# Optimization experiments

Measured on AMD Instinct MI355X. Metric: run time of the kernel, lower is better.

## Reference

```python
import jax, jax.numpy as jnp
import numpy as np

V, E, H, T = 50000, 1024, 1024, 128
L, MAXL = 50, 50
PAD, O_TOK = 0, 1


def setup_inputs() -> dict:
    key = jax.random.key(0)
    ks = jax.random.split(key, 18)
    s = 0.05
    f = lambda k, shape: jax.random.normal(k, shape, jnp.float32) * s
    return {
        'input_ids': jax.random.randint(ks[0], (1, L), 1, V),
        'tag_ids': jax.random.randint(ks[1], (1, L), 1, T),  # >=1 so no pad tags
        'word_embed': f(ks[2], (V, E)),
        'enc_Wih': f(ks[3], (3 * H, E)),
        'enc_Whh': f(ks[4], (3 * H, H)),
        'enc_bih': f(ks[5], (3 * H,)),
        'enc_bhh': f(ks[6], (3 * H,)),
        'dec_embed': f(ks[7], (T, H)),
        'attn_W': f(ks[8], (MAXL, 2 * H)),
        'attn_b': f(ks[9], (MAXL,)),
        'comb_W': f(ks[10], (H, 2 * H)),
        'comb_b': f(ks[11], (H,)),
        'dec_Wih': f(ks[12], (3 * H, H)),
        'dec_Whh': f(ks[13], (3 * H, H)),
        'dec_bih': f(ks[14], (3 * H,)),
        'dec_bhh': f(ks[15], (3 * H,)),
        'out_W': f(ks[16], (T, H)),
        'out_b': f(ks[17], (T,)),
    }


def _gru_cell(x, h, Wih, Whh, bih, bhh):
    # PyTorch GRU cell semantics
    gi = Wih @ x + bih
    gh = Whh @ h + bhh
    i_r, i_z, i_n = jnp.split(gi, 3)
    h_r, h_z, h_n = jnp.split(gh, 3)
    r = jax.nn.sigmoid(i_r + h_r)
    z = jax.nn.sigmoid(i_z + h_z)
    n = jnp.tanh(i_n + r * h_n)
    return (1.0 - z) * n + z * h


def _forward(word_embed, enc_Wih, enc_Whh, enc_bih, enc_bhh,
             dec_embed, attn_W, attn_b, comb_W, comb_b,
             dec_Wih, dec_Whh, dec_bih, dec_bhh, out_W, out_b,
             input_ids, tag_ids):
    src = input_ids[0]  # (L,)
    tgt = tag_ids[0]    # (L,)

    def enc_step(h, tok):
        h2 = _gru_cell(word_embed[tok], h, enc_Wih, enc_Whh, enc_bih, enc_bhh)
        return h2, h2

    h_enc, enc_outs = jax.lax.scan(enc_step, jnp.zeros((H,), word_embed.dtype), src)
    # enc_outs: (L, H); L == MAX_LENGTH so the buffer is fully filled

    dec_in = jnp.concatenate([jnp.array([O_TOK], tgt.dtype), tgt[:-1]])  # teacher forcing

    def dec_step(h, xt):
        tok, tgt_t = xt
        e = dec_embed[tok]  # (H,), dropout is identity in eval
        aw = jax.nn.softmax(attn_W @ jnp.concatenate([e, h]) + attn_b)  # (MAXL,)
        ctx = aw @ enc_outs  # (H,)
        o = jax.nn.relu(comb_W @ jnp.concatenate([e, ctx]) + comb_b)
        h2 = _gru_cell(o, h, dec_Wih, dec_Whh, dec_bih, dec_bhh)
        logp = jax.nn.log_softmax(out_W @ h2 + out_b)  # decoder output (log-probs)
        # original applies CrossEntropyLoss on log-probs -> log_softmax applied twice
        nll = -jax.nn.log_softmax(logp)[tgt_t]
        step_loss = jnp.where(tgt_t == PAD, jnp.zeros((), logp.dtype), nll)
        return h2, (logp, step_loss)

    _, (logps, losses) = jax.lax.scan(dec_step, h_enc, (dec_in, tgt))
    return logps, jnp.sum(losses)  # (L, T), scalar


def reference(input_ids, tag_ids, word_embed, enc_Wih, enc_Whh, enc_bih, enc_bhh,
              dec_embed, attn_W, attn_b, comb_W, comb_b,
              dec_Wih, dec_Whh, dec_bih, dec_bhh, out_W, out_b):
    return _forward(word_embed, enc_Wih, enc_Whh, enc_bih, enc_bhh,
                    dec_embed, attn_W, attn_b, comb_W, comb_b,
                    dec_Wih, dec_Whh, dec_bih, dec_bhh, out_W, out_b,
                    input_ids, tag_ids)
```

## Files before the change

### kernel.cpp

```cpp
#include <hip/hip_runtime.h>
#include <cstdint>


#define HDIM 1024
#define LSEQ 50
#define TDIM 128
#define PB   6
#define NPROD 128
#define LSTRP 65

typedef float f32x4 __attribute__((ext_vector_type(4)));
typedef _Float16 h2 __attribute__((ext_vector_type(2)));

#if __has_builtin(__builtin_amdgcn_fdot2)
#define FDOT2(a,b,c) __builtin_amdgcn_fdot2((a),(b),(c),false)
#else
__device__ __forceinline__ float fdot2_sw(h2 a, h2 b, float c){
  return c + (float)a[0]*(float)b[0] + (float)a[1]*(float)b[1];
}
#define FDOT2(a,b,c) fdot2_sw((a),(b),(c))
#endif

struct KArgs {
  const int* input_ids; const int* tag_ids;
  const float* word_embed;
  const float* enc_Wih; const float* enc_Whh; const float* enc_bih; const float* enc_bhh;
  const float* dec_embed; const float* attn_W; const float* attn_b;
  const float* comb_W; const float* comb_b;
  const float* dec_Wih; const float* dec_Whh; const float* dec_bih; const float* dec_bhh;
  const float* out_W; const float* out_b;
  float* out;
  unsigned* ctrM; unsigned* ctrO; unsigned* ctrV;
  float* hbE;
  float* hbD;
  float* obD;
  float* logits;
  float* enc_outs;
  float* attn_e;
  float* pre_comb;
  float* MT;
};

__device__ __forceinline__ void fence_vm(){
  asm volatile("s_waitcnt vmcnt(0)" ::: "memory");
}
__device__ __forceinline__ void st_coh(float* p, float v){
  __hip_atomic_store(p, v, __ATOMIC_RELAXED, __HIP_MEMORY_SCOPE_AGENT);
}
__device__ __forceinline__ void st_tag(float* p, float v, unsigned tag){
  unsigned b = (__float_as_uint(v) & ~31u) | tag;
  st_coh(p, __uint_as_float(b));
}
__device__ __forceinline__ void stf(unsigned* p, unsigned v){
  __hip_atomic_store(p, v, __ATOMIC_RELAXED, __HIP_MEMORY_SCOPE_AGENT);
}
__device__ __forceinline__ unsigned ldu(const unsigned* p){
  return __hip_atomic_load(p, __ATOMIC_RELAXED, __HIP_MEMORY_SCOPE_AGENT);
}
__device__ __forceinline__ void addc0(unsigned* base){
  __hip_atomic_fetch_add(base, 1u, __ATOMIC_RELAXED, __HIP_MEMORY_SCOPE_AGENT);
}
__device__ __forceinline__ f32x4 coh_load4(const float* p){
  f32x4 v;
  asm volatile("global_load_dwordx4 %0, %1, off sc0 sc1\n\ts_waitcnt vmcnt(0)"
               : "=v"(v) : "v"(p) : "memory");
  return v;
}

template<int N>
__device__ __forceinline__ void wred_batch(float* v){
  #pragma unroll
  for(int o=32;o>0;o>>=1){
    #pragma unroll
    for(int i=0;i<N;i++) v[i] += __shfl_xor(v[i],o,64);
  }
}
__device__ __forceinline__ float wred_sum(float v){
  #pragma unroll
  for(int o=32;o>0;o>>=1) v += __shfl_xor(v,o,64);
  return v;
}
__device__ __forceinline__ float wred_max(float v){
  #pragma unroll
  for(int o=32;o>0;o>>=1) v = fmaxf(v,__shfl_xor(v,o,64));
  return v;
}

__device__ __forceinline__ void load_vec16(const float* __restrict__ v, float* hc, int lane){
  const f32x4* p = reinterpret_cast<const f32x4*>(v) + lane*4;
  f32x4 x0=p[0],x1=p[1],x2=p[2],x3=p[3];
  hc[0]=x0.x; hc[1]=x0.y; hc[2]=x0.z; hc[3]=x0.w;
  hc[4]=x1.x; hc[5]=x1.y; hc[6]=x1.z; hc[7]=x1.w;
  hc[8]=x2.x; hc[9]=x2.y; hc[10]=x2.z; hc[11]=x2.w;
  hc[12]=x3.x; hc[13]=x3.y; hc[14]=x3.z; hc[15]=x3.w;
}

struct PChunk { unsigned m[8]; };
__device__ __forceinline__ h2 as_h2(unsigned u){ return __builtin_bit_cast(h2, u); }
__device__ __forceinline__ unsigned as_u(h2 h){ return __builtin_bit_cast(unsigned, h); }
__device__ __forceinline__ unsigned pack2(float a, float b){
  return as_u((h2){(_Float16)a, (_Float16)b});
}
__device__ __forceinline__ PChunk load_pchunk(const float* __restrict__ row, int lane){
  const f32x4* p = reinterpret_cast<const f32x4*>(row) + lane*4;
  f32x4 a=p[0],b=p[1],c=p[2],d=p[3];
  PChunk w;
  w.m[0]=pack2(a.x,a.y); w.m[1]=pack2(a.z,a.w);
  w.m[2]=pack2(b.x,b.y); w.m[3]=pack2(b.z,b.w);
  w.m[4]=pack2(c.x,c.y); w.m[5]=pack2(c.z,c.w);
  w.m[6]=pack2(d.x,d.y); w.m[7]=pack2(d.z,d.w);
  return w;
}
__device__ __forceinline__ void pinp(PChunk& c){
  asm volatile("" : "+v"(c.m[0]),"+v"(c.m[1]),"+v"(c.m[2]),"+v"(c.m[3]),
                    "+v"(c.m[4]),"+v"(c.m[5]),"+v"(c.m[6]),"+v"(c.m[7]));
}
__device__ __forceinline__ void pin32(unsigned& x){ asm volatile("" : "+v"(x)); }
__device__ __forceinline__ float pdot(const PChunk& w, const h2* hp){
  float acc = 0.f;
  #pragma unroll
  for(int k=0;k<8;k++) acc = FDOT2(as_h2(w.m[k]), hp[k], acc);
  return acc;
}
__device__ __forceinline__ float sigm(float x){ return 1.f/(1.f+expf(-x)); }
__device__ __forceinline__ void pack16(const float* ec, h2* ep){
  #pragma unroll
  for(int k=0;k<8;k++) ep[k]=(h2){(_Float16)ec[2*k],(_Float16)ec[2*k+1]};
}

template<int SLP>
__device__ __forceinline__ void stage_tag_p(h2* ldsp, const float* g, int tid, unsigned tag){
  const float* p = g + 4*tid;
  f32x4 v;
  for(;;){
    v = coh_load4(p);
    unsigned m = ((__float_as_uint(v.x)&31u)^tag) | ((__float_as_uint(v.y)&31u)^tag)
               | ((__float_as_uint(v.z)&31u)^tag) | ((__float_as_uint(v.w)&31u)^tag);
    if(m==0u) break;
    if(SLP) __builtin_amdgcn_s_sleep(SLP);
  }
  int q = tid>>2, m0 = (tid&3)*2;
  ldsp[m0*LSTRP+q]     = (h2){(_Float16)v.x,(_Float16)v.y};
  ldsp[(m0+1)*LSTRP+q] = (h2){(_Float16)v.z,(_Float16)v.w};
}
__device__ __forceinline__ void read8p(const h2* ldsp, h2* hp, int lane){
  #pragma unroll
  for(int k=0;k<8;k++) hp[k]=ldsp[k*LSTRP+lane];
}
__device__ __forceinline__ float hread(const h2* ldsp, int j){
  int pj = j>>1;
  h2 v = ldsp[(pj&7)*LSTRP + (pj>>3)];
  return (float)v[j&1];
}

__device__ __forceinline__ void wait2_enc(const float* g, unsigned tg, int lane){
  const float* p0 = g + lane*16 + 7;
  const float* p1 = g + lane*16 + 15;
  for(;;){
    float a,b;
    asm volatile("global_load_dword %0, %2, off sc0 sc1\n\t"
                 "global_load_dword %1, %3, off sc0 sc1\n\t"
                 "s_waitcnt vmcnt(0)"
                 : "=v"(a), "=v"(b) : "v"(p0), "v"(p1) : "memory");
    unsigned m = ((__float_as_uint(a)&31u)^tg) | ((__float_as_uint(b)&31u)^tg);
    if(__all((int)(m==0u))) return;
    __builtin_amdgcn_s_sleep(4);
  }
}
__device__ __forceinline__ void load16_tag(const float* g, unsigned tg, int lane, h2* ep){
  const float* p = g + lane*16;
  for(;;){
    f32x4 a=coh_load4(p), b=coh_load4(p+4), c=coh_load4(p+8), d=coh_load4(p+12);
    unsigned m = ((__float_as_uint(a.x)&31u)^tg)|((__float_as_uint(a.y)&31u)^tg)
               | ((__float_as_uint(a.z)&31u)^tg)|((__float_as_uint(a.w)&31u)^tg)
               | ((__float_as_uint(b.x)&31u)^tg)|((__float_as_uint(b.y)&31u)^tg)
               | ((__float_as_uint(b.z)&31u)^tg)|((__float_as_uint(b.w)&31u)^tg)
               | ((__float_as_uint(c.x)&31u)^tg)|((__float_as_uint(c.y)&31u)^tg)
               | ((__float_as_uint(c.z)&31u)^tg)|((__float_as_uint(c.w)&31u)^tg)
               | ((__float_as_uint(d.x)&31u)^tg)|((__float_as_uint(d.y)&31u)^tg)
               | ((__float_as_uint(d.z)&31u)^tg)|((__float_as_uint(d.w)&31u)^tg);
    if(m==0u){
      ep[0]=(h2){(_Float16)a.x,(_Float16)a.y}; ep[1]=(h2){(_Float16)a.z,(_Float16)a.w};
      ep[2]=(h2){(_Float16)b.x,(_Float16)b.y}; ep[3]=(h2){(_Float16)b.z,(_Float16)b.w};
      ep[4]=(h2){(_Float16)c.x,(_Float16)c.y}; ep[5]=(h2){(_Float16)c.z,(_Float16)c.w};
      ep[6]=(h2){(_Float16)d.x,(_Float16)d.y}; ep[7]=(h2){(_Float16)d.z,(_Float16)d.w};
      return;
    }
    __builtin_amdgcn_s_sleep(2);
  }
}

__global__ __launch_bounds__(256,1) void seq2seq_kernel(KArgs A){
  const int bid = blockIdx.x, tid = threadIdx.x;
  const int wave = tid>>6, lane = tid&63;
  __shared__ h2 ldsp_h[8*LSTRP+8];
  __shared__ h2 ldsp_o[8*LSTRP+8];
  __shared__ h2 awpL[32];
  __shared__ float smr[64];
  __shared__ float smL[TDIM];
  __shared__ float smA[64];
  __shared__ float giL[LSEQ*24];

  const int p = bid - PB;
  const bool is_prod = (p>=0 && p<NPROD);
  const int base = is_prod ? p*8 : 0;
  const int j8 = base + (tid&7);

  if(is_prod){
    {
      PChunk wgi[6]; float bgi[6];
      #pragma unroll
      for(int i=0;i<6;i++){
        int r = wave + 4*i;
        int le=r/3, g=r-3*le, grow=g*HDIM+base+le;
        wgi[i] = load_pchunk(A.enc_Wih + (size_t)grow*HDIM, lane);
        pinp(wgi[i]);
        bgi[i] = A.enc_bih[grow];
      }
      for(int te=0;te<LSEQ;++te){
        int tok = A.input_ids[te];
        float ec[16]; load_vec16(A.word_embed + (size_t)tok*HDIM, ec, lane);
        h2 ep[8]; pack16(ec, ep);
        float d[6];
        #pragma unroll
        for(int i=0;i<6;i++) d[i]=pdot(wgi[i],ep);
        wred_batch<6>(d);
        if(lane==0){
          #pragma unroll
          for(int i=0;i<6;i++) giL[te*24 + wave+4*i] = d[i]+bgi[i];
        }
      }
      __syncthreads();
    }
    PChunk wep[6];
    #pragma unroll
    for(int i=0;i<6;i++){
      int r = wave + 4*i;
      int le=r/3, g=r-3*le, row=g*HDIM+base+le;
      wep[i] = load_pchunk(A.enc_Whh + (size_t)row*HDIM, lane);
      pinp(wep[i]);
    }
    float bh0=A.enc_bhh[j8], bh1=A.enc_bhh[HDIM+j8], bh2=A.enc_bhh[2*HDIM+j8];
    for(int te=0;te<LSEQ;++te){
      h2 hp[8];
      if(te>0){
        stage_tag_p<1>(ldsp_h, A.hbE + ((te-1)&1)*HDIM, tid, (unsigned)(te&31));
        __syncthreads();
        read8p(ldsp_h, hp, lane);
      } else {
        #pragma unroll
        for(int k=0;k<8;k++) hp[k]=(h2){(_Float16)0.f,(_Float16)0.f};
      }
      float part[6];
      #pragma unroll
      for(int i=0;i<6;i++) part[i]=pdot(wep[i],hp);
      wred_batch<6>(part);
      if(lane==0){
        #pragma unroll
        for(int i=0;i<6;i++) smr[wave+4*i]=part[i];
      }
      __syncthreads();
      if(tid<8){
        int j = base+tid;
        float gr=smr[tid*3]+bh0, gz=smr[tid*3+1]+bh1, gn=smr[tid*3+2]+bh2;
        float gi0=giL[te*24+3*tid], gi1=giL[te*24+3*tid+1], gi2=giL[te*24+3*tid+2];
        float hj = (te>0)? hread(ldsp_h, j) : 0.f;
        float r_=sigm(gi0+gr), z_=sigm(gi1+gz);
        float n_=tanhf(gi2+r_*gn);
        float h2v=(1.f-z_)*n_+z_*hj;
        st_tag(&A.hbE[(te&1)*HDIM+j], h2v, (unsigned)((te+1)&31));
        st_tag(&A.enc_outs[te*HDIM+j], h2v, (unsigned)(te%31));
        if(te==LSEQ-1) st_tag(&A.hbD[j], h2v, 0u);
      }
      __syncthreads();
    }
    fence_vm();
    __syncthreads();
  } else {
    const int q = (bid<6)? bid : bid-128;
    PChunk wpc[2]; float bpc[2]; int ri[2];
    #pragma unroll
    for(int k=0;k<2;k++){
      ri[k] = q*8 + wave*2 + k;
      wpc[k] = load_pchunk(A.comb_W + (size_t)ri[k]*2*HDIM, lane);
      pinp(wpc[k]);
      bpc[k] = A.comb_b[ri[k]];
    }
    for(int t=0;t<LSEQ;++t){
      int tok = (t==0)?1:A.tag_ids[t-1];
      float ec[16]; load_vec16(A.dec_embed + (size_t)tok*HDIM, ec, lane);
      h2 ep[8]; pack16(ec, ep);
      float d[2] = {pdot(wpc[0],ep), pdot(wpc[1],ep)};
      wred_batch<2>(d);
      if(lane==0){
        st_coh(&A.pre_comb[t*HDIM+ri[0]], d[0]+bpc[0]);
        st_coh(&A.pre_comb[t*HDIM+ri[1]], d[1]+bpc[1]);
      }
    }
    if(q < LSEQ){
      PChunk wae = load_pchunk(A.attn_W + (size_t)q*2*HDIM, lane);
      float bae = A.attn_b[q];
      const int t0 = wave*13, tc = (wave<3)?13:11;
      for(int u=0;u<tc;++u){
        int t = t0+u;
        int tok = (t==0)?1:A.tag_ids[t-1];
        float ec[16]; load_vec16(A.dec_embed + (size_t)tok*HDIM, ec, lane);
        h2 ep[8]; pack16(ec, ep);
        float d = wred_sum(pdot(wae,ep));
        if(lane==0) st_coh(&A.attn_e[t*LSEQ+q], d+bae);
      }
    }
    {
      const int si = q*4 + wave;
      PChunk wm0 = load_pchunk(A.comb_W + (size_t)si*2*HDIM + HDIM, lane);
      pinp(wm0);
      PChunk wm1 = load_pchunk(A.comb_W + (size_t)(si+512)*2*HDIM + HDIM, lane);
      pinp(wm1);
      for(int s=0;s<LSEQ;++s){
        const unsigned tg = (unsigned)(s%31);
        const float* g = A.enc_outs + s*HDIM;
        wait2_enc(g, tg, lane);
        h2 ep[8]; load16_tag(g, tg, lane, ep);
        float dd[2] = {pdot(wm0,ep), pdot(wm1,ep)};
        wred_batch<2>(dd);
        if(lane==0){
          st_coh(&A.MT[s*HDIM+si],     dd[0]);
          st_coh(&A.MT[s*HDIM+si+512], dd[1]);
        }
      }
    }
    fence_vm();
    __syncthreads();
    if(tid==0) addc0(A.ctrM);
  }

  if(bid < 4){
    const int oi = bid*256 + tid;
    PChunk wa13[13];
    int srow[13];
    #pragma unroll
    for(int i=0;i<13;i++){
      int s = wave + 4*i; int sc = (s<LSEQ)? s : 0;
      wa13[i] = load_pchunk(A.attn_W + (size_t)sc*2*HDIM + HDIM, lane);
      pinp(wa13[i]);
      srow[i] = s;
    }
    if(wave==0){
      for(;;){
        unsigned v = (lane==0)? ldu(A.ctrM) : 128u;
        if(__all((int)(v>=128u))) break;
        __builtin_amdgcn_s_sleep(2);
      }
    }
    __syncthreads();
    unsigned mp[25];
    #pragma unroll
    for(int k=0;k<25;k++){
      mp[k] = pack2(A.MT[(2*k)*HDIM+oi], A.MT[(2*k+1)*HDIM+oi]);
      pin32(mp[k]);
    }
    for(int t=0;t<LSEQ;++t){
      const unsigned tg = (unsigned)(t&31);
      float ae[13];
      #pragma unroll
      for(int i=0;i<13;i++)
        ae[i] = (srow[i]<LSEQ)? A.attn_e[t*LSEQ+srow[i]] : 0.f;
      float pcv = A.pre_comb[t*HDIM+oi];
      stage_tag_p<1>(ldsp_h, A.hbD + (t%3)*HDIM, tid, tg);
      __syncthreads();
      h2 hp[8]; read8p(ldsp_h, hp, lane);
      float pl[13];
      #pragma unroll
      for(int i=0;i<13;i++) pl[i]=pdot(wa13[i],hp);
      wred_batch<13>(pl);
      if(lane==0){
        #pragma unroll
        for(int i=0;i<13;i++) if(srow[i]<LSEQ) smL[srow[i]]=pl[i]+ae[i];
      }
      __syncthreads();
      if(wave==0){
        float l = (lane<LSEQ)? smL[lane] : -1e30f;
        float m = wred_max(l);
        float pe = (lane<LSEQ)? expf(l-m) : 0.f;
        float ss = wred_sum(pe);
        if(lane<LSEQ) smA[lane] = pe/ss;
      }
      __syncthreads();
      if(tid<25) awpL[tid] = (h2){(_Float16)smA[2*tid],(_Float16)smA[2*tid+1]};
      __syncthreads();
      float acc = pcv;
      #pragma unroll
      for(int k=0;k<25;k++) acc = FDOT2(as_h2(mp[k]), awpL[k], acc);
      st_tag(&A.obD[(t&1)*HDIM+oi], fmaxf(acc,0.f), tg);
      __syncthreads();
    }
  } else if(bid == 4){
    float loss = 0.f;
    for(int t=0;t<LSEQ;++t){
      if(tid<32){
        const float* pp = A.logits + (t&1)*TDIM + 4*tid;
        const unsigned tg = (unsigned)(t&31);
        f32x4 v;
        for(;;){
          v = coh_load4(pp);
          unsigned m = ((__float_as_uint(v.x)&31u)^tg) | ((__float_as_uint(v.y)&31u)^tg)
                     | ((__float_as_uint(v.z)&31u)^tg) | ((__float_as_uint(v.w)&31u)^tg);
          if(m==0u) break;
          __builtin_amdgcn_s_sleep(2);
        }
        smL[4*tid]=v.x; smL[4*tid+1]=v.y; smL[4*tid+2]=v.z; smL[4*tid+3]=v.w;
      }
      __syncthreads();
      if(tid==0) stf(A.ctrV, (unsigned)(t+1));
      if(wave==0){
        float l0=smL[lane], l1=smL[lane+64];
        float m  = wred_max(fmaxf(l0,l1));
        float pe = expf(l0-m)+expf(l1-m);
        float s1 = wred_sum(pe);
        float lse = m + logf(s1);
        float lp0 = l0-lse, lp1 = l1-lse;
        float m2  = wred_max(fmaxf(lp0,lp1));
        float p2  = expf(lp0-m2)+expf(lp1-m2);
        float s2  = wred_sum(p2);
        float lse2 = m2 + logf(s2);
        A.out[t*TDIM + lane]      = lp0;
        A.out[t*TDIM + 64 + lane] = lp1;
        int tg2 = A.tag_ids[t];
        float c = ((lane==tg2)?(lse2-lp0):0.f) + ((lane+64==tg2)?(lse2-lp1):0.f);
        c = wred_sum(c);
        if(tg2 != 0) loss += c;
      }
      __syncthreads();
    }
    if(tid==0) A.out[LSEQ*TDIM] = loss;
  } else if(is_prod){
    PChunk whp[6], wip[6];
    #pragma unroll
    for(int i=0;i<6;i++){
      int r = wave + 4*i;
      int le=r/3, g=r-3*le, row=g*HDIM+base+le;
      whp[i] = load_pchunk(A.dec_Whh + (size_t)row*HDIM, lane);
      pinp(whp[i]);
      wip[i] = load_pchunk(A.dec_Wih + (size_t)row*HDIM, lane);
      pinp(wip[i]);
    }
    float dh0=A.dec_bhh[j8], dh1=A.dec_bhh[HDIM+j8], dh2=A.dec_bhh[2*HDIM+j8];
    float di0=A.dec_bih[j8], di1=A.dec_bih[HDIM+j8], di2=A.dec_bih[2*HDIM+j8];
    for(int t=0;t<LSEQ;++t){
      const unsigned tg = (unsigned)(t&31);
      stage_tag_p<1>(ldsp_h, A.hbD + (t%3)*HDIM, tid, tg);
      __syncthreads();
      h2 hp[8]; read8p(ldsp_h, hp, lane);
      float ph[6];
      #pragma unroll
      for(int i=0;i<6;i++) ph[i]=pdot(whp[i],hp);
      wred_batch<6>(ph);
      if(lane==0){
        #pragma unroll
        for(int i=0;i<6;i++) smr[wave+4*i]=ph[i];
      }
      if(wave==0 && t>=3){
        const unsigned tgt = 16u*(unsigned)(t-2);
        for(;;){
          unsigned v = (lane==0)? ldu(A.ctrO) : tgt;
          if(__all((int)(v>=tgt))) break;
          __builtin_amdgcn_s_sleep(2);
        }
      }
      stage_tag_p<1>(ldsp_o, A.obD + (t&1)*HDIM, tid, tg);
      __syncthreads();
      h2 op[8]; read8p(ldsp_o, op, lane);
      float po[6];
      #pragma unroll
      for(int i=0;i<6;i++) po[i]=pdot(wip[i],op);
      wred_batch<6>(po);
      if(lane==0){
        #pragma unroll
        for(int i=0;i<6;i++) smr[32+wave+4*i]=po[i];
      }
      __syncthreads();
      if(tid<8){
        int j = base+tid;
        float gr=smr[tid*3]+dh0,    gz=smr[tid*3+1]+dh1,    gn=smr[tid*3+2]+dh2;
        float ir=smr[32+tid*3]+di0, iz=smr[32+tid*3+1]+di1, inn=smr[32+tid*3+2]+di2;
        float hj = hread(ldsp_h, j);
        float r_=sigm(ir+gr), z_=sigm(iz+gz);
        float n_=tanhf(inn+r_*gn);
        float h2v=(1.f-z_)*n_+z_*hj;
        st_tag(&A.hbD[((t+1)%3)*HDIM+j], h2v, (unsigned)((t+1)&31));
      }
      __syncthreads();
    }
  } else if(bid>=134 && bid<150){
    const int ob = bid-134;
    PChunk wop[2];
    float bo[2];
    #pragma unroll
    for(int i=0;i<2;i++){
      int row = ob*8 + wave*2 + i;
      wop[i]=load_pchunk(A.out_W+(size_t)row*HDIM,lane);
      pinp(wop[i]);
      bo[i]=A.out_b[row];
    }
    for(int t=0;t<LSEQ;++t){
      const unsigned tg1 = (unsigned)((t+1)&31);
      stage_tag_p<2>(ldsp_h, A.hbD + ((t+1)%3)*HDIM, tid, tg1);
      __syncthreads();
      if(tid==0) addc0(A.ctrO);
      h2 hp[8]; read8p(ldsp_h, hp, lane);
      float pt[2]={pdot(wop[0],hp),pdot(wop[1],hp)};
      wred_batch<2>(pt);
      if(wave==0 && t>=2){
        const unsigned tgt = (unsigned)(t-1);
        for(;;){
          unsigned v = (lane==0)? ldu(A.ctrV) : tgt;
          if(__all((int)(v>=tgt))) break;
          __builtin_amdgcn_s_sleep(4);
        }
      }
      __syncthreads();
      if(lane==0){
        int row = ob*8 + wave*2;
        st_tag(&A.logits[(t&1)*TDIM + row],   pt[0]+bo[0], (unsigned)(t&31));
        st_tag(&A.logits[(t&1)*TDIM + row+1], pt[1]+bo[1], (unsigned)(t&31));
      }
      __syncthreads();
    }
  }
}

extern "C" void kernel_launch(void* const* d_in, const int* in_sizes, int n_in,
                              void* d_out, int out_size, void* d_ws, size_t ws_size,
                              hipStream_t stream){
  (void)in_sizes; (void)n_in; (void)out_size; (void)ws_size;
  KArgs A;
  A.input_ids = (const int*)d_in[0];
  A.tag_ids   = (const int*)d_in[1];
  A.word_embed= (const float*)d_in[2];
  A.enc_Wih   = (const float*)d_in[3];
  A.enc_Whh   = (const float*)d_in[4];
  A.enc_bih   = (const float*)d_in[5];
  A.enc_bhh   = (const float*)d_in[6];
  A.dec_embed = (const float*)d_in[7];
  A.attn_W    = (const float*)d_in[8];
  A.attn_b    = (const float*)d_in[9];
  A.comb_W    = (const float*)d_in[10];
  A.comb_b    = (const float*)d_in[11];
  A.dec_Wih   = (const float*)d_in[12];
  A.dec_Whh   = (const float*)d_in[13];
  A.dec_bih   = (const float*)d_in[14];
  A.dec_bhh   = (const float*)d_in[15];
  A.out_W     = (const float*)d_in[16];
  A.out_b     = (const float*)d_in[17];
  A.out       = (float*)d_out;

  unsigned* u = (unsigned*)d_ws;
  A.ctrM = u;
  A.ctrO = u + 64;
  A.ctrV = u + 128;
  float* f = (float*)d_ws + 1024;
  A.hbE      = f; f += 2*HDIM;
  A.hbD      = f; f += 3*HDIM;
  A.obD      = f; f += 2*HDIM;
  A.logits   = f; f += 2*TDIM;
  A.enc_outs = f; f += LSEQ*HDIM;
  A.attn_e   = f; f += LSEQ*LSEQ + 14;
  A.pre_comb = f; f += LSEQ*HDIM;
  A.MT       = f; f += LSEQ*HDIM;

  (void)hipMemsetAsync(d_ws, 0, 4096, stream);
  (void)hipMemsetAsync((char*)d_ws + 4096, 0xFF, 58624*4, stream);
  void* args[] = { &A };
  hipError_t err = hipLaunchCooperativeKernel((const void*)seq2seq_kernel,
                                              dim3(256), dim3(256), args, 0, stream);
  if(err != hipSuccess){
    hipLaunchKernelGGL(seq2seq_kernel, dim3(256), dim3(256), 0, stream, A);
  }
}
```

Baseline: 458.8 us.

## Compute attention combine redundantly in producer blocks, publish only softmax weights

Four attention blocks used to compute the full combined vector and publish it through global memory for every decoder step. Now a single block computes only the 50 softmax attention weights and publishes them. Each of the 128 producer blocks loads the full MT matrix into registers and recomputes the whole combined vector locally. This drops one global round trip and the 4-block fan-in from the per-step critical path. The cost is redundant work and much higher register pressure in the producers (100 pinned registers per thread). A new counter lets the attention block start once attn_e is ready, before MT is finished.

```diff
diff --git a/kernel.cpp b/kernel.cpp
--- a/kernel.cpp
+++ b/kernel.cpp
@@ -30,11 +30,11 @@
   const float* dec_Wih; const float* dec_Whh; const float* dec_bih; const float* dec_bhh;
   const float* out_W; const float* out_b;
   float* out;
-  unsigned* ctrM; unsigned* ctrO; unsigned* ctrV;
+  unsigned* ctrA; unsigned* ctrM; unsigned* ctrO; unsigned* ctrV;
   float* hbE;
   float* hbD;
-  float* obD;
   float* logits;
+  float* awb;
   float* enc_outs;
   float* attn_e;
   float* pre_comb;
@@ -189,6 +189,13 @@
     __builtin_amdgcn_s_sleep(2);
   }
 }
+__device__ __forceinline__ void wait_ctr1(const unsigned* p, unsigned n, int lane){
+  for(;;){
+    unsigned v = (lane==0)? ldu(p) : n;
+    if(__all((int)(v>=n))) return;
+    __builtin_amdgcn_s_sleep(2);
+  }
+}
 
 __global__ __launch_bounds__(256,1) void seq2seq_kernel(KArgs A){
   const int bid = blockIdx.x, tid = threadIdx.x;
@@ -310,6 +317,9 @@
         if(lane==0) st_coh(&A.attn_e[t*LSEQ+q], d+bae);
       }
     }
+    fence_vm();
+    __syncthreads();
+    if(tid==0) addc0(A.ctrA);
     {
       const int si = q*4 + wave;
       PChunk wm0 = load_pchunk(A.comb_W + (size_t)si*2*HDIM + HDIM, lane);
@@ -334,8 +344,7 @@
     if(tid==0) addc0(A.ctrM);
   }
 
-  if(bid < 4){
-    const int oi = bid*256 + tid;
+  if(bid == 0){
     PChunk wa13[13];
     int srow[13];
     #pragma unroll
@@ -345,28 +354,15 @@
       pinp(wa13[i]);
       srow[i] = s;
     }
-    if(wave==0){
-      for(;;){
-        unsigned v = (lane==0)? ldu(A.ctrM) : 128u;
-        if(__all((int)(v>=128u))) break;
-        __builtin_amdgcn_s_sleep(2);
-      }
-    }
+    if(wave==0) wait_ctr1(A.ctrA, 128u, lane);
     __syncthreads();
-    unsigned mp[25];
-    #pragma unroll
-    for(int k=0;k<25;k++){
-      mp[k] = pack2(A.MT[(2*k)*HDIM+oi], A.MT[(2*k+1)*HDIM+oi]);
-      pin32(mp[k]);
-    }
     for(int t=0;t<LSEQ;++t){
       const unsigned tg = (unsigned)(t&31);
       float ae[13];
       #pragma unroll
       for(int i=0;i<13;i++)
         ae[i] = (srow[i]<LSEQ)? A.attn_e[t*LSEQ+srow[i]] : 0.f;
-      float pcv = A.pre_comb[t*HDIM+oi];
-      stage_tag_p<1>(ldsp_h, A.hbD + (t%3)*HDIM, tid, tg);
+      stage_tag_p<0>(ldsp_h, A.hbD + (t%3)*HDIM, tid, tg);
       __syncthreads();
       h2 hp[8]; read8p(ldsp_h, hp, lane);
       float pl[13];
@@ -383,15 +379,9 @@
         float m = wred_max(l);
         float pe = (lane<LSEQ)? expf(l-m) : 0.f;
         float ss = wred_sum(pe);
-        if(lane<LSEQ) smA[lane] = pe/ss;
-      }
-      __syncthreads();
-      if(tid<25) awpL[tid] = (h2){(_Float16)smA[2*tid],(_Float16)smA[2*tid+1]};
-      __syncthreads();
-      float acc = pcv;
-      #pragma unroll
-      for(int k=0;k<25;k++) acc = FDOT2(as_h2(mp[k]), awpL[k], acc);
-      st_tag(&A.obD[(t&1)*HDIM+oi], fmaxf(acc,0.f), tg);
+        float av = (lane<LSEQ)? pe/ss : 0.f;
+        if(lane<52) st_tag(&A.awb[(t&1)*64+lane], av, tg);
+      }
       __syncthreads();
     }
   } else if(bid == 4){
@@ -446,8 +436,23 @@
     }
     float dh0=A.dec_bhh[j8], dh1=A.dec_bhh[HDIM+j8], dh2=A.dec_bhh[2*HDIM+j8];
     float di0=A.dec_bih[j8], di1=A.dec_bih[HDIM+j8], di2=A.dec_bih[2*HDIM+j8];
+    if(wave==0) wait_ctr1(A.ctrM, 128u, lane);
+    __syncthreads();
+    unsigned mp0[25], mp1[25], mp2[25], mp3[25];
+    {
+      const int j0 = 4*tid;
+      #pragma unroll
+      for(int k=0;k<25;k++){
+        mp0[k]=pack2(A.MT[(2*k)*HDIM+j0  ], A.MT[(2*k+1)*HDIM+j0  ]); pin32(mp0[k]);
+        mp1[k]=pack2(A.MT[(2*k)*HDIM+j0+1], A.MT[(2*k+1)*HDIM+j0+1]); pin32(mp1[k]);
+        mp2[k]=pack2(A.MT[(2*k)*HDIM+j0+2], A.MT[(2*k+1)*HDIM+j0+2]); pin32(mp2[k]);
+        mp3[k]=pack2(A.MT[(2*k)*HDIM+j0+3], A.MT[(2*k+1)*HDIM+j0+3]); pin32(mp3[k]);
+      }
+    }
+    const f32x4* PC4 = reinterpret_cast<const f32x4*>(A.pre_comb);
     for(int t=0;t<LSEQ;++t){
       const unsigned tg = (unsigned)(t&31);
+      f32x4 pc = PC4[t*256+tid];
       stage_tag_p<1>(ldsp_h, A.hbD + (t%3)*HDIM, tid, tg);
       __syncthreads();
       h2 hp[8]; read8p(ldsp_h, hp, lane);
@@ -467,7 +472,35 @@
           __builtin_amdgcn_s_sleep(2);
         }
       }
-      stage_tag_p<1>(ldsp_o, A.obD + (t&1)*HDIM, tid, tg);
+      if(tid<13){
+        const float* pp = A.awb + (t&1)*64 + 4*tid;
+        f32x4 v;
+        for(;;){
+          v = coh_load4(pp);
+          unsigned m = ((__float_as_uint(v.x)&31u)^tg) | ((__float_as_uint(v.y)&31u)^tg)
+                     | ((__float_as_uint(v.z)&31u)^tg) | ((__float_as_uint(v.w)&31u)^tg);
+          if(m==0u) break;
+          __builtin_amdgcn_s_sleep(1);
+        }
+        smA[4*tid]=v.x; smA[4*tid+1]=v.y; smA[4*tid+2]=v.z; smA[4*tid+3]=v.w;
+      }
+      __syncthreads();
+      if(tid<25) awpL[tid] = (h2){(_Float16)smA[2*tid],(_Float16)smA[2*tid+1]};
+      __syncthreads();
+      {
+        float o0=pc.x, o1=pc.y, o2=pc.z, o3=pc.w;
+        #pragma unroll
+        for(int k=0;k<25;k++){
+          h2 aw = awpL[k];
+          o0 = FDOT2(as_h2(mp0[k]), aw, o0);
+          o1 = FDOT2(as_h2(mp1[k]), aw, o1);
+          o2 = FDOT2(as_h2(mp2[k]), aw, o2);
+          o3 = FDOT2(as_h2(mp3[k]), aw, o3);
+        }
+        int q = tid>>2, m0 = (tid&3)*2;
+        ldsp_o[m0*LSTRP+q]     = (h2){(_Float16)fmaxf(o0,0.f),(_Float16)fmaxf(o1,0.f)};
+        ldsp_o[(m0+1)*LSTRP+q] = (h2){(_Float16)fmaxf(o2,0.f),(_Float16)fmaxf(o3,0.f)};
+      }
       __syncthreads();
       h2 op[8]; read8p(ldsp_o, op, lane);
       float po[6];
@@ -555,21 +588,22 @@
   A.out       = (float*)d_out;
 
   unsigned* u = (unsigned*)d_ws;
-  A.ctrM = u;
-  A.ctrO = u + 64;
-  A.ctrV = u + 128;
+  A.ctrA = u;
+  A.ctrM = u + 64;
+  A.ctrO = u + 128;
+  A.ctrV = u + 192;
   float* f = (float*)d_ws + 1024;
   A.hbE      = f; f += 2*HDIM;
   A.hbD      = f; f += 3*HDIM;
-  A.obD      = f; f += 2*HDIM;
   A.logits   = f; f += 2*TDIM;
+  A.awb      = f; f += 2*64;
   A.enc_outs = f; f += LSEQ*HDIM;
   A.attn_e   = f; f += LSEQ*LSEQ + 14;
   A.pre_comb = f; f += LSEQ*HDIM;
   A.MT       = f; f += LSEQ*HDIM;
 
   (void)hipMemsetAsync(d_ws, 0, 4096, stream);
-  (void)hipMemsetAsync((char*)d_ws + 4096, 0xFF, 58624*4, stream);
+  (void)hipMemsetAsync((char*)d_ws + 4096, 0xFF, 56704*4, stream);
   void* args[] = { &A };
   hipError_t err = hipLaunchCooperativeKernel((const void*)seq2seq_kernel,
                                               dim3(256), dim3(256), args, 0, stream);
```

New measurement: 457.4 us. About the same (-0.3%).
